# Optimization experiments

Measured on AMD Instinct MI355X. Metric: run time of the kernel, lower is better.

The kernel has to match this reference:

```python
import jax, jax.numpy as jnp
import numpy as np


def _pair_indices(num_emb):
    # pair (i, j), i != j; torch builds pair vector = concat(emb[j], emb[i])
    ii, jj = np.meshgrid(np.arange(num_emb), np.arange(num_emb), indexing='ij')
    mask = ii != jj
    return jnp.asarray(ii[mask]), jnp.asarray(jj[mask])


def setup_inputs() -> dict:
    key = jax.random.key(0)
    ks = jax.random.split(key, 8)
    B, n_way, n_shot, n_query, F = 64, 2, 6, 16, 512
    s = 0.02
    return {
        'x_shot_feat': jax.random.normal(ks[0], (B * n_way * n_shot, F), jnp.float32),
        'x_query_feat': jax.random.normal(ks[1], (B * n_query, F), jnp.float32),
        'Wg1': jax.random.normal(ks[2], (2 * F, F), jnp.float32) * s,
        'bg1': jnp.zeros((F,), jnp.float32),
        'Wg2': jax.random.normal(ks[3], (F, F), jnp.float32) * s,
        'bg2': jnp.zeros((F,), jnp.float32),
        'Wf1': jax.random.normal(ks[4], (F, F), jnp.float32) * s,
        'bf1': jnp.zeros((F,), jnp.float32),
        'Wf2': jax.random.normal(ks[5], (F, 1), jnp.float32) * s,
        'bf2': jnp.zeros((1,), jnp.float32),
        'batch_size': B, 'n_way': n_way, 'n_shot': n_shot, 'n_query': n_query,
    }


def reference(x_shot_feat, x_query_feat, Wg1, bg1, Wg2, bg2, Wf1, bf1, Wf2, bf2,
              batch_size, n_way, n_shot, n_query):
    F = x_shot_feat.shape[-1]
    num_emb = n_shot + 1
    x_shot = x_shot_feat.reshape(batch_size, n_way, n_shot, F)
    pos, neg = x_shot[:, 0], x_shot[:, 1]          # [B, n_shot, F]
    q = x_query_feat.reshape(batch_size, n_query, F)

    # emb: [B, Q, way=2, num_emb, F]  (support set + the single query appended)
    shot = jnp.stack([pos, neg], axis=1)           # [B, 2, n_shot, F]
    shot_b = jnp.broadcast_to(shot[:, None], (batch_size, n_query, 2, n_shot, F))
    q_b = jnp.broadcast_to(q[:, :, None, None, :], (batch_size, n_query, 2, 1, F))
    emb = jnp.concatenate([shot_b, q_b], axis=3)   # [B, Q, 2, num_emb, F]

    idx_i, idx_j = _pair_indices(num_emb)          # P = num_emb^2 - num_emb
    # pair(i,j) = concat(emb[j], emb[i])  (matches torch expand order)
    pairs = jnp.concatenate([emb[..., idx_j, :], emb[..., idx_i, :]], axis=-1)  # [B,Q,2,P,2F]

    g = jax.nn.relu(pairs @ Wg1 + bg1)
    g = jax.nn.relu(g @ Wg2 + bg2)                 # [B, Q, 2, P, F]
    s = jnp.sum(g, axis=3)                         # [B, Q, 2, F]
    logit = jax.nn.relu(s @ Wf1 + bf1) @ Wf2 + bf2 # [B, Q, 2, 1]
    return logit[..., 0]                           # [B, Q, n_way]
```

## Files before the change

kernel.cpp:

```cpp
#include <hip/hip_runtime.h>
#include <stdint.h>

typedef _Float16 f16x8 __attribute__((ext_vector_type(8)));
typedef float f32x4 __attribute__((ext_vector_type(4)));

__device__ __forceinline__ void gload16(const void* g, void* l) {
  __builtin_amdgcn_global_load_lds((const __attribute__((address_space(1))) void*)g,
                                   (__attribute__((address_space(3))) void*)l,
                                   16, 0, 0);
}

__device__ __forceinline__ void maprow_ss(int gr, int& rowU, int& rowV, bool& ok) {
  int g = gr >> 5, p = gr & 31;
  ok = (p < 30);
  int i = p / 5, jj = p % 5;
  int j = jj + (jj >= i);
  rowU = g * 6 + j;
  rowV = g * 6 + i;
  if (!ok) { rowU = 0; rowV = 0; }
}

__device__ __forceinline__ void maprow_sq(int gr, int& rowU, int& rowV) {
  int h = gr / 12, p = gr % 12;
  int b = h >> 5, q = (h >> 1) & 15, wv = h & 1;
  int sbase = (b * 2 + wv) * 6;
  int qrow = 768 + b * 16 + q;
  if (p < 6) { rowU = qrow; rowV = sbase + p; }
  else       { rowU = sbase + (p - 6); rowV = qrow; }
}

__device__ __forceinline__ f16x8 cvt8h(float4 a, float4 b) {
  f16x8 o;
  o[0] = (_Float16)a.x; o[1] = (_Float16)a.y; o[2] = (_Float16)a.z; o[3] = (_Float16)a.w;
  o[4] = (_Float16)b.x; o[5] = (_Float16)b.y; o[6] = (_Float16)b.z; o[7] = (_Float16)b.w;
  return o;
}

__global__ void convert_t(const float* __restrict__ Wg1, const float* __restrict__ Wg2,
                          const float* __restrict__ Wf1, const float* __restrict__ bf2,
                          _Float16* __restrict__ Wg1T, _Float16* __restrict__ Wg2T,
                          _Float16* __restrict__ Wf1T, float* __restrict__ out) {
  int tt = blockIdx.x * 256 + threadIdx.x;
  if (tt < 2048) out[tt] = bf2[0];
  const float* src;
  _Float16* dst;
  int c, k0, scol, srow0;
  if (tt < 65536) {
    c = tt & 1023; k0 = (tt >> 10) << 3;
    dst = Wg1T + (size_t)c * 512 + k0;
    if (c < 512) { src = Wg1; scol = c; srow0 = k0; }
    else         { src = Wg1; scol = c - 512; srow0 = 512 + k0; }
  } else if (tt < 98304) {
    int t2 = tt - 65536;
    c = t2 & 511; k0 = (t2 >> 9) << 3;
    dst = Wg2T + (size_t)c * 512 + k0;
    src = Wg2; scol = c; srow0 = k0;
  } else {
    int t3 = tt - 98304;
    c = t3 & 511; k0 = (t3 >> 9) << 3;
    dst = Wf1T + (size_t)c * 512 + k0;
    src = Wf1; scol = c; srow0 = k0;
  }
  f16x8 o;
#pragma unroll
  for (int i = 0; i < 8; i++)
    o[i] = (_Float16)src[(size_t)(srow0 + i) * 512 + scol];
  *(f16x8*)dst = o;
}

__global__ __launch_bounds__(256, 2) void gemm1_fused(
    const float* __restrict__ xs, const float* __restrict__ xq,
    const _Float16* __restrict__ BT, const float* __restrict__ bg1,
    _Float16* __restrict__ UVh) {
  __shared__ __align__(16) char smem[24576];

  int bid = blockIdx.x;
  { int q = gridDim.x >> 3; bid = (bid & 7) * q + (bid >> 3); }
  const int tm = bid >> 4;
  const int tn = bid & 15;
  const int t = threadIdx.x, w = t >> 6, l = t & 63;
  const int wm = (w >> 1) << 6, wn = (w & 1) << 5;
  const int lr = l & 15, lg = l >> 4;

  const int rl0 = t >> 2, c = t & 3;
  const int wchunk = c ^ ((rl0 >> 2) & 3);
  const int gr0 = tm * 128 + rl0, gr1 = gr0 + 64;
  const float* x0 = ((gr0 < 768) ? xs + (size_t)gr0 * 512 : xq + (size_t)(gr0 - 768) * 512) + c * 8;
  const float* x1 = ((gr1 < 768) ? xs + (size_t)gr1 * 512 : xq + (size_t)(gr1 - 768) * 512) + c * 8;

  const int kch = ((t & 3) ^ ((t >> 4) & 3)) * 8;
  const _Float16* Bg = BT + (size_t)(tn * 64 + rl0) * 512 + kch;

  _Float16* As_base = (_Float16*)smem;
  char*     Bs_base = smem + 16384;

  f32x4 acc[4][2];
#pragma unroll
  for (int m = 0; m < 4; m++)
#pragma unroll
    for (int n = 0; n < 2; n++) acc[m][n] = (f32x4){0.f, 0.f, 0.f, 0.f};
  const int rchunk = (lg ^ (lr >> 2)) * 8;

  gload16(Bg, Bs_base + t * 16);
  {
    float4 a0 = *(const float4*)(x0), a1 = *(const float4*)(x0 + 4);
    float4 b0 = *(const float4*)(x1), b1 = *(const float4*)(x1 + 4);
    *(f16x8*)(As_base + rl0 * 32 + wchunk * 8) = cvt8h(a0, a1);
    *(f16x8*)(As_base + (rl0 + 64) * 32 + wchunk * 8) = cvt8h(b0, b1);
  }
  __syncthreads();

  int cur = 0;
  for (int it = 0; it < 15; ++it) {
    const int nxt = cur ^ 1;
    const int kn = (it + 1) * 32;
    gload16(Bg + kn, Bs_base + nxt * 4096 + t * 16);
    float4 a0 = *(const float4*)(x0 + kn), a1 = *(const float4*)(x0 + kn + 4);
    float4 b0 = *(const float4*)(x1 + kn), b1 = *(const float4*)(x1 + kn + 4);
    {
      _Float16* As = As_base + cur * 4096;
      _Float16* Bs = (_Float16*)(Bs_base + cur * 4096);
      f16x8 fa[4], fb[2];
#pragma unroll
      for (int m = 0; m < 4; m++)
        fa[m] = *(const f16x8*)(As + (wm + m * 16 + lr) * 32 + rchunk);
#pragma unroll
      for (int n = 0; n < 2; n++)
        fb[n] = *(const f16x8*)(Bs + (wn + n * 16 + lr) * 32 + rchunk);
#pragma unroll
      for (int m = 0; m < 4; m++)
#pragma unroll
        for (int n = 0; n < 2; n++)
          acc[m][n] = __builtin_amdgcn_mfma_f32_16x16x32_f16(fa[m], fb[n], acc[m][n], 0, 0, 0);
    }
    *(f16x8*)(As_base + nxt * 4096 + rl0 * 32 + wchunk * 8) = cvt8h(a0, a1);
    *(f16x8*)(As_base + nxt * 4096 + (rl0 + 64) * 32 + wchunk * 8) = cvt8h(b0, b1);
    __syncthreads();
    cur = nxt;
  }
  {
    _Float16* As = As_base + cur * 4096;
    _Float16* Bs = (_Float16*)(Bs_base + cur * 4096);
    f16x8 fa[4], fb[2];
#pragma unroll
    for (int m = 0; m < 4; m++)
      fa[m] = *(const f16x8*)(As + (wm + m * 16 + lr) * 32 + rchunk);
#pragma unroll
    for (int n = 0; n < 2; n++)
      fb[n] = *(const f16x8*)(Bs + (wn + n * 16 + lr) * 32 + rchunk);
#pragma unroll
    for (int m = 0; m < 4; m++)
#pragma unroll
      for (int n = 0; n < 2; n++)
        acc[m][n] = __builtin_amdgcn_mfma_f32_16x16x32_f16(fa[m], fb[n], acc[m][n], 0, 0, 0);
  }

#pragma unroll
  for (int m = 0; m < 4; m++)
#pragma unroll
    for (int n = 0; n < 2; n++) {
      int col = tn * 64 + wn + n * 16 + lr;
      float bv = (col >= 512) ? bg1[col - 512] : 0.0f;
#pragma unroll
      for (int reg = 0; reg < 4; reg++) {
        int row = tm * 128 + wm + m * 16 + lg * 4 + reg;
        UVh[(size_t)row * 1024 + col] = (_Float16)(acc[m][n][reg] + bv);
      }
    }
}

__global__ __launch_bounds__(256, 2) void gemm2_fused(
    const _Float16* __restrict__ UVh,
    const _Float16* __restrict__ BT, const float* __restrict__ bg2,
    float* __restrict__ outSS, float* __restrict__ outSQ) {
  __shared__ __align__(16) char smem[32768];

  int bid = blockIdx.x;
  { int q = gridDim.x >> 3; bid = (bid & 7) * q + (bid >> 3); }
  const int t = threadIdx.x, w = t >> 6, l = t & 63;
  const int lr = l & 15, lg = l >> 4;
  const int rl = t >> 2, c = t & 3;
  const int wchunk = c ^ ((t >> 4) & 3);
  const int kch = ((t & 3) ^ ((t >> 4) & 3)) * 8;
  const int rchunk = (lg ^ (lr >> 2)) * 8;
  const f16x8 zz = {};
  char* Bsb = smem + 16384;

  if (bid < 1024) {
    const int tile = bid >> 2, tn = bid & 3;
    const int wm = (w >> 1) * 48, wn = (w & 1) << 6;

    int rU0, rV0, rU1 = 0, rV1 = 0;
    maprow_sq(tile * 96 + rl, rU0, rV0);
    if (t < 128) maprow_sq(tile * 96 + 64 + rl, rU1, rV1);
    const _Float16* u0p = UVh + (size_t)rU0 * 1024 + c * 8;
    const _Float16* v0p = UVh + (size_t)rV0 * 1024 + 512 + c * 8;
    const _Float16* u1p = UVh + (size_t)rU1 * 1024 + c * 8;
    const _Float16* v1p = UVh + (size_t)rV1 * 1024 + 512 + c * 8;
    const _Float16* Bg = BT + (size_t)(tn * 128 + rl) * 512 + kch;

    f32x4 acc[3][4];
#pragma unroll
    for (int m = 0; m < 3; m++)
#pragma unroll
      for (int n = 0; n < 4; n++) acc[m][n] = (f32x4){0.f, 0.f, 0.f, 0.f};

    {
      f16x8 u0 = *(const f16x8*)(u0p), v0 = *(const f16x8*)(v0p);
      *(f16x8*)((_Float16*)smem + rl * 32 + wchunk * 8) =
          __builtin_elementwise_max(u0 + v0, zz);
      if (t < 128) {
        f16x8 u1 = *(const f16x8*)(u1p), v1 = *(const f16x8*)(v1p);
        *(f16x8*)((_Float16*)smem + (64 + rl) * 32 + wchunk * 8) =
            __builtin_elementwise_max(u1 + v1, zz);
      }
    }
    gload16(Bg, Bsb + t * 16);
    gload16(Bg + (size_t)64 * 512, Bsb + 4096 + t * 16);
    __syncthreads();

    int cur = 0;
    for (int it = 0; it < 15; ++it) {
      const int nxt = cur ^ 1;
      const int kn = (it + 1) * 32;
      gload16(Bg + kn, Bsb + nxt * 8192 + t * 16);
      gload16(Bg + (size_t)64 * 512 + kn, Bsb + nxt * 8192 + 4096 + t * 16);
      f16x8 u0 = *(const f16x8*)(u0p + kn), v0 = *(const f16x8*)(v0p + kn);
      f16x8 u1, v1;
      if (t < 128) { u1 = *(const f16x8*)(u1p + kn); v1 = *(const f16x8*)(v1p + kn); }
      {
        _Float16* As = (_Float16*)(smem + cur * 6144);
        _Float16* Bs = (_Float16*)(Bsb + cur * 8192);
        f16x8 fa[3], fb[4];
#pragma unroll
        for (int m = 0; m < 3; m++)
          fa[m] = *(const f16x8*)(As + (wm + m * 16 + lr) * 32 + rchunk);
#pragma unroll
        for (int n = 0; n < 4; n++)
          fb[n] = *(const f16x8*)(Bs + (wn + n * 16 + lr) * 32 + rchunk);
#pragma unroll
        for (int m = 0; m < 3; m++)
#pragma unroll
          for (int n = 0; n < 4; n++)
            acc[m][n] = __builtin_amdgcn_mfma_f32_16x16x32_f16(fa[m], fb[n], acc[m][n], 0, 0, 0);
      }
      {
        _Float16* Aw = (_Float16*)(smem + nxt * 6144);
        *(f16x8*)(Aw + rl * 32 + wchunk * 8) = __builtin_elementwise_max(u0 + v0, zz);
        if (t < 128)
          *(f16x8*)(Aw + (64 + rl) * 32 + wchunk * 8) = __builtin_elementwise_max(u1 + v1, zz);
      }
      __syncthreads();
      cur = nxt;
    }
    {
      _Float16* As = (_Float16*)(smem + cur * 6144);
      _Float16* Bs = (_Float16*)(Bsb + cur * 8192);
      f16x8 fa[3], fb[4];
#pragma unroll
      for (int m = 0; m < 3; m++)
        fa[m] = *(const f16x8*)(As + (wm + m * 16 + lr) * 32 + rchunk);
#pragma unroll
      for (int n = 0; n < 4; n++)
        fb[n] = *(const f16x8*)(Bs + (wn + n * 16 + lr) * 32 + rchunk);
#pragma unroll
      for (int m = 0; m < 3; m++)
#pragma unroll
        for (int n = 0; n < 4; n++)
          acc[m][n] = __builtin_amdgcn_mfma_f32_16x16x32_f16(fa[m], fb[n], acc[m][n], 0, 0, 0);
    }
    __syncthreads();

    float* scr = (float*)smem + w * 192;
#pragma unroll
    for (int n = 0; n < 4; n++) {
      int col = tn * 128 + wn + n * 16 + lr;
      float bv = bg2[col];
#pragma unroll
      for (int m = 0; m < 3; m++) {
        float s = 0.0f;
#pragma unroll
        for (int reg = 0; reg < 4; reg++)
          s += fmaxf(acc[m][n][reg] + bv, 0.0f);
        scr[(4 * m + lg) * 16 + lr] = s;
      }
#pragma unroll
      for (int g = 0; g < 4; g++) {
        float vs = scr[(3 * g) * 16 + lr] + scr[(3 * g + 1) * 16 + lr] +
                   scr[(3 * g + 2) * 16 + lr];
        if (l < 16) {
          int hh = tile * 8 + ((wm == 48) ? 4 : 0) + g;
          outSQ[(size_t)hh * 512 + col] = vs;
        }
      }
    }
  } else {
    const int sbid = bid - 1024;
    const int tm = sbid >> 2, tn = sbid & 3;
    const int wm = (w >> 1) << 6, wn = (w & 1) << 6;

    int rU0, rV0, rU1, rV1; bool ok0, ok1;
    maprow_ss(tm * 128 + rl, rU0, rV0, ok0);
    maprow_ss(tm * 128 + rl + 64, rU1, rV1, ok1);
    const _Float16* u0p = UVh + (size_t)rU0 * 1024 + c * 8;
    const _Float16* v0p = UVh + (size_t)rV0 * 1024 + 512 + c * 8;
    const _Float16* u1p = UVh + (size_t)rU1 * 1024 + c * 8;
    const _Float16* v1p = UVh + (size_t)rV1 * 1024 + 512 + c * 8;
    const _Float16* Bg = BT + (size_t)(tn * 128 + rl) * 512 + kch;

    f32x4 acc[4][4];
#pragma unroll
    for (int m = 0; m < 4; m++)
#pragma unroll
      for (int n = 0; n < 4; n++) acc[m][n] = (f32x4){0.f, 0.f, 0.f, 0.f};

    {
      f16x8 u0 = *(const f16x8*)(u0p), v0 = *(const f16x8*)(v0p);
      f16x8 u1 = *(const f16x8*)(u1p), v1 = *(const f16x8*)(v1p);
      f16x8 o0 = ok0 ? __builtin_elementwise_max(u0 + v0, zz) : zz;
      f16x8 o1 = ok1 ? __builtin_elementwise_max(u1 + v1, zz) : zz;
      *(f16x8*)((_Float16*)smem + rl * 32 + wchunk * 8) = o0;
      *(f16x8*)((_Float16*)smem + (rl + 64) * 32 + wchunk * 8) = o1;
    }
    gload16(Bg, Bsb + t * 16);
    gload16(Bg + (size_t)64 * 512, Bsb + 4096 + t * 16);
    __syncthreads();

    int cur = 0;
    for (int it = 0; it < 15; ++it) {
      const int nxt = cur ^ 1;
      const int kn = (it + 1) * 32;
      gload16(Bg + kn, Bsb + nxt * 8192 + t * 16);
      gload16(Bg + (size_t)64 * 512 + kn, Bsb + nxt * 8192 + 4096 + t * 16);
      f16x8 u0 = *(const f16x8*)(u0p + kn), v0 = *(const f16x8*)(v0p + kn);
      f16x8 u1 = *(const f16x8*)(u1p + kn), v1 = *(const f16x8*)(v1p + kn);
      {
        _Float16* As = (_Float16*)(smem + cur * 8192);
        _Float16* Bs = (_Float16*)(Bsb + cur * 8192);
        f16x8 fa[4], fb[4];
#pragma unroll
        for (int m = 0; m < 4; m++)
          fa[m] = *(const f16x8*)(As + (wm + m * 16 + lr) * 32 + rchunk);
#pragma unroll
        for (int n = 0; n < 4; n++)
          fb[n] = *(const f16x8*)(Bs + (wn + n * 16 + lr) * 32 + rchunk);
#pragma unroll
        for (int m = 0; m < 4; m++)
#pragma unroll
          for (int n = 0; n < 4; n++)
            acc[m][n] = __builtin_amdgcn_mfma_f32_16x16x32_f16(fa[m], fb[n], acc[m][n], 0, 0, 0);
      }
      {
        f16x8 o0 = ok0 ? __builtin_elementwise_max(u0 + v0, zz) : zz;
        f16x8 o1 = ok1 ? __builtin_elementwise_max(u1 + v1, zz) : zz;
        _Float16* Aw = (_Float16*)(smem + nxt * 8192);
        *(f16x8*)(Aw + rl * 32 + wchunk * 8) = o0;
        *(f16x8*)(Aw + (rl + 64) * 32 + wchunk * 8) = o1;
      }
      __syncthreads();
      cur = nxt;
    }
    {
      _Float16* As = (_Float16*)(smem + cur * 8192);
      _Float16* Bs = (_Float16*)(Bsb + cur * 8192);
      f16x8 fa[4], fb[4];
#pragma unroll
      for (int m = 0; m < 4; m++)
        fa[m] = *(const f16x8*)(As + (wm + m * 16 + lr) * 32 + rchunk);
#pragma unroll
      for (int n = 0; n < 4; n++)
        fb[n] = *(const f16x8*)(Bs + (wn + n * 16 + lr) * 32 + rchunk);
#pragma unroll
      for (int m = 0; m < 4; m++)
#pragma unroll
        for (int n = 0; n < 4; n++)
          acc[m][n] = __builtin_amdgcn_mfma_f32_16x16x32_f16(fa[m], fb[n], acc[m][n], 0, 0, 0);
    }

#pragma unroll
    for (int pair = 0; pair < 2; pair++) {
#pragma unroll
      for (int n = 0; n < 4; n++) {
        int col = tn * 128 + wn + n * 16 + lr;
        float bv = bg2[col];
        float s = 0.0f;
#pragma unroll
        for (int mh = 0; mh < 2; mh++) {
          int m = pair * 2 + mh;
#pragma unroll
          for (int reg = 0; reg < 4; reg++) {
            bool ok = (mh == 0) || (lg * 4 + reg < 14);
            float v = fmaxf(acc[m][n][reg] + bv, 0.0f);
            s += ok ? v : 0.0f;
          }
        }
        s += __shfl_xor(s, 16);
        s += __shfl_xor(s, 32);
        if (l < 16) {
          int g = (wm >> 5) + pair;
          outSS[(size_t)(tm * 4 + g) * 512 + col] = s;
        }
      }
    }
  }
}

__global__ __launch_bounds__(256, 2) void gemm3_fused(
    const float* __restrict__ SS, const float* __restrict__ SQ,
    const _Float16* __restrict__ BT, const float* __restrict__ bf1,
    const float* __restrict__ Wf2, float* __restrict__ out) {
  __shared__ __align__(16) char smem[24576];

  int bid = blockIdx.x;
  { int q = gridDim.x >> 3; bid = (bid & 7) * q + (bid >> 3); }
  const int tm = bid >> 3;
  const int tn = bid & 7;
  const int t = threadIdx.x, w = t >> 6, l = t & 63;
  const int wm = (w >> 1) << 6, wn = (w & 1) << 5;
  const int lr = l & 15, lg = l >> 4;

  const int rl0 = t >> 2, c = t & 3;
  const int wchunk = c ^ ((rl0 >> 2) & 3);
  const int gr0 = tm * 128 + rl0, gr1 = gr0 + 64;
  const int ss0 = (gr0 >> 5) * 2 + (gr0 & 1);
  const int ss1 = (gr1 >> 5) * 2 + (gr1 & 1);
  const float* s0p = SS + (size_t)ss0 * 512 + c * 8;
  const float* q0p = SQ + (size_t)gr0 * 512 + c * 8;
  const float* s1p = SS + (size_t)ss1 * 512 + c * 8;
  const float* q1p = SQ + (size_t)gr1 * 512 + c * 8;

  const int kch = ((t & 3) ^ ((t >> 4) & 3)) * 8;
  const _Float16* Bg = BT + (size_t)(tn * 64 + rl0) * 512 + kch;

  _Float16* As_base = (_Float16*)smem;
  char*     Bs_base = smem + 16384;

  f32x4 acc[4][2];
#pragma unroll
  for (int m = 0; m < 4; m++)
#pragma unroll
    for (int n = 0; n < 2; n++) acc[m][n] = (f32x4){0.f, 0.f, 0.f, 0.f};
  const int rchunk = (lg ^ (lr >> 2)) * 8;

#define BUILD_S(o, a0, a1, b0, b1)                                           \
  {                                                                          \
    o[0] = (_Float16)(a0.x + b0.x); o[1] = (_Float16)(a0.y + b0.y);          \
    o[2] = (_Float16)(a0.z + b0.z); o[3] = (_Float16)(a0.w + b0.w);          \
    o[4] = (_Float16)(a1.x + b1.x); o[5] = (_Float16)(a1.y + b1.y);          \
    o[6] = (_Float16)(a1.z + b1.z); o[7] = (_Float16)(a1.w + b1.w);          \
  }

  gload16(Bg, Bs_base + t * 16);
  {
    float4 a0 = *(const float4*)(s0p), a1 = *(const float4*)(s0p + 4);
    float4 b0 = *(const float4*)(q0p), b1 = *(const float4*)(q0p + 4);
    float4 c0 = *(const float4*)(s1p), c1 = *(const float4*)(s1p + 4);
    float4 d0 = *(const float4*)(q1p), d1 = *(const float4*)(q1p + 4);
    f16x8 o0, o1;
    BUILD_S(o0, a0, a1, b0, b1);
    BUILD_S(o1, c0, c1, d0, d1);
    *(f16x8*)(As_base + rl0 * 32 + wchunk * 8) = o0;
    *(f16x8*)(As_base + (rl0 + 64) * 32 + wchunk * 8) = o1;
  }
  __syncthreads();

  int cur = 0;
  for (int it = 0; it < 15; ++it) {
    const int nxt = cur ^ 1;
    const int kn = (it + 1) * 32;
    gload16(Bg + kn, Bs_base + nxt * 4096 + t * 16);
    float4 a0 = *(const float4*)(s0p + kn), a1 = *(const float4*)(s0p + kn + 4);
    float4 b0 = *(const float4*)(q0p + kn), b1 = *(const float4*)(q0p + kn + 4);
    float4 c0 = *(const float4*)(s1p + kn), c1 = *(const float4*)(s1p + kn + 4);
    float4 d0 = *(const float4*)(q1p + kn), d1 = *(const float4*)(q1p + kn + 4);
    {
      _Float16* As = As_base + cur * 4096;
      _Float16* Bs = (_Float16*)(Bs_base + cur * 4096);
      f16x8 fa[4], fb[2];
#pragma unroll
      for (int m = 0; m < 4; m++)
        fa[m] = *(const f16x8*)(As + (wm + m * 16 + lr) * 32 + rchunk);
#pragma unroll
      for (int n = 0; n < 2; n++)
        fb[n] = *(const f16x8*)(Bs + (wn + n * 16 + lr) * 32 + rchunk);
#pragma unroll
      for (int m = 0; m < 4; m++)
#pragma unroll
        for (int n = 0; n < 2; n++)
          acc[m][n] = __builtin_amdgcn_mfma_f32_16x16x32_f16(fa[m], fb[n], acc[m][n], 0, 0, 0);
    }
    {
      f16x8 o0, o1;
      BUILD_S(o0, a0, a1, b0, b1);
      BUILD_S(o1, c0, c1, d0, d1);
      *(f16x8*)(As_base + nxt * 4096 + rl0 * 32 + wchunk * 8) = o0;
      *(f16x8*)(As_base + nxt * 4096 + (rl0 + 64) * 32 + wchunk * 8) = o1;
    }
    __syncthreads();
    cur = nxt;
  }
  {
    _Float16* As = As_base + cur * 4096;
    _Float16* Bs = (_Float16*)(Bs_base + cur * 4096);
    f16x8 fa[4], fb[2];
#pragma unroll
    for (int m = 0; m < 4; m++)
      fa[m] = *(const f16x8*)(As + (wm + m * 16 + lr) * 32 + rchunk);
#pragma unroll
    for (int n = 0; n < 2; n++)
      fb[n] = *(const f16x8*)(Bs + (wn + n * 16 + lr) * 32 + rchunk);
#pragma unroll
    for (int m = 0; m < 4; m++)
#pragma unroll
      for (int n = 0; n < 2; n++)
        acc[m][n] = __builtin_amdgcn_mfma_f32_16x16x32_f16(fa[m], fb[n], acc[m][n], 0, 0, 0);
  }

  float bf1v[2], wf2v[2];
#pragma unroll
  for (int n = 0; n < 2; n++) {
    int col = tn * 64 + wn + n * 16 + lr;
    bf1v[n] = bf1[col];
    wf2v[n] = Wf2[col];
  }
#pragma unroll
  for (int m = 0; m < 4; m++) {
#pragma unroll
    for (int reg = 0; reg < 4; reg++) {
      float p = 0.0f;
#pragma unroll
      for (int n = 0; n < 2; n++)
        p += fmaxf(acc[m][n][reg] + bf1v[n], 0.0f) * wf2v[n];
      p += __shfl_xor(p, 1);
      p += __shfl_xor(p, 2);
      p += __shfl_xor(p, 4);
      p += __shfl_xor(p, 8);
      if (lr == 0) {
        int row = tm * 128 + wm + m * 16 + lg * 4 + reg;
        atomicAdd(&out[row], p);
      }
    }
  }
#undef BUILD_S
}

extern "C" void kernel_launch(void* const* d_in, const int* in_sizes, int n_in,
                              void* d_out, int out_size, void* d_ws, size_t ws_size,
                              hipStream_t stream) {
  const float* xs  = (const float*)d_in[0];
  const float* xq  = (const float*)d_in[1];
  const float* Wg1 = (const float*)d_in[2];
  const float* bg1 = (const float*)d_in[3];
  const float* Wg2 = (const float*)d_in[4];
  const float* bg2 = (const float*)d_in[5];
  const float* Wf1 = (const float*)d_in[6];
  const float* bf1 = (const float*)d_in[7];
  const float* Wf2 = (const float*)d_in[8];
  const float* bf2 = (const float*)d_in[9];
  float* out = (float*)d_out;

  char* ws = (char*)d_ws;
  _Float16* Wg1T = (_Float16*)(ws);
  _Float16* Wg2T = (_Float16*)(ws + 1048576);
  _Float16* Wf1T = (_Float16*)(ws + 1572864);
  _Float16* UVh  = (_Float16*)(ws + 2097152);
  float*    SSs  = (float*)(ws + 5767168);
  float*    SQs  = (float*)(ws + 6029312);

  convert_t<<<512, 256, 0, stream>>>(Wg1, Wg2, Wf1, bf2, Wg1T, Wg2T, Wf1T, out);
  gemm1_fused<<<224, 256, 0, stream>>>(xs, xq, Wg1T, bg1, UVh);
  gemm2_fused<<<1152, 256, 0, stream>>>(UVh, Wg2T, bg2, SSs, SQs);
  gemm3_fused<<<128, 256, 0, stream>>>(SSs, SQs, Wf1T, bf1, Wf2, out);
}
```

Baseline: 71.93 us.

## Split gemm2 into separate SQ and SS kernels; build SQ A-fragments in registers

Splits the fused gemm2 kernel into two launches, one for support-query pairs and one for support-support pairs. In the SQ kernel each lane now loads its U and V rows straight into MFMA A-fragment registers and applies add+ReLU there, so the A tile no longer goes through LDS. The loads are prefetched one K-step ahead and a manual vmcnt/barrier sequence replaces __syncthreads. This cuts LDS traffic and halves the LDS footprint of the SQ path, which may improve occupancy. In exchange the two kernels now run back to back instead of sharing one grid, which adds a launch and a tail, and the hand-written waitcnt counts have to match the number of outstanding loads exactly.

```diff
diff --git a/kernel.cpp b/kernel.cpp
--- a/kernel.cpp
+++ b/kernel.cpp
@@ -169,16 +169,131 @@
     }
 }
 
-__global__ __launch_bounds__(256, 2) void gemm2_fused(
+__global__ __launch_bounds__(256, 2) void gemm2_sq(
     const _Float16* __restrict__ UVh,
     const _Float16* __restrict__ BT, const float* __restrict__ bg2,
-    float* __restrict__ outSS, float* __restrict__ outSQ) {
-  __shared__ __align__(16) char smem[32768];
+    float* __restrict__ outSQ) {
+  __shared__ __align__(16) char smem[16384];
 
   int bid = blockIdx.x;
   { int q = gridDim.x >> 3; bid = (bid & 7) * q + (bid >> 3); }
+  const int tile = bid >> 2, tn = bid & 3;
   const int t = threadIdx.x, w = t >> 6, l = t & 63;
   const int lr = l & 15, lg = l >> 4;
+  const int wm = (w >> 1) * 48, wn = (w & 1) << 6;
+  const int rl = t >> 2;
+  const int kch = ((t & 3) ^ ((t >> 4) & 3)) * 8;
+  const int rchunk = (lg ^ (lr >> 2)) * 8;
+  const f16x8 zz = {};
+
+  const _Float16 *uf[3], *vf[3];
+#pragma unroll
+  for (int m = 0; m < 3; m++) {
+    int rU, rV;
+    maprow_sq(tile * 96 + wm + m * 16 + lr, rU, rV);
+    uf[m] = UVh + (size_t)rU * 1024 + lg * 8;
+    vf[m] = UVh + (size_t)rV * 1024 + 512 + lg * 8;
+  }
+  const _Float16* Bg = BT + (size_t)(tn * 128 + rl) * 512 + kch;
+
+  f32x4 acc[3][4];
+#pragma unroll
+  for (int m = 0; m < 3; m++)
+#pragma unroll
+    for (int n = 0; n < 4; n++) acc[m][n] = (f32x4){0.f, 0.f, 0.f, 0.f};
+
+  gload16(Bg, smem + t * 16);
+  gload16(Bg + (size_t)64 * 512, smem + 4096 + t * 16);
+  f16x8 uc[3], vc[3];
+#pragma unroll
+  for (int m = 0; m < 3; m++) { uc[m] = *(const f16x8*)(uf[m]); vc[m] = *(const f16x8*)(vf[m]); }
+  asm volatile("s_waitcnt vmcnt(6) lgkmcnt(0)" ::: "memory");
+  __builtin_amdgcn_s_barrier();
+  asm volatile("" ::: "memory");
+
+  for (int it = 0; it < 15; ++it) {
+    const int kn = (it + 1) * 32;
+    const int nxt = (it + 1) & 1;
+    gload16(Bg + kn, smem + nxt * 8192 + t * 16);
+    gload16(Bg + (size_t)64 * 512 + kn, smem + nxt * 8192 + 4096 + t * 16);
+    f16x8 un[3], vn[3];
+#pragma unroll
+    for (int m = 0; m < 3; m++) { un[m] = *(const f16x8*)(uf[m] + kn); vn[m] = *(const f16x8*)(vf[m] + kn); }
+    {
+      _Float16* Bs = (_Float16*)(smem + (it & 1) * 8192);
+      f16x8 fb[4];
+#pragma unroll
+      for (int n = 0; n < 4; n++)
+        fb[n] = *(const f16x8*)(Bs + (wn + n * 16 + lr) * 32 + rchunk);
+      f16x8 fa[3];
+#pragma unroll
+      for (int m = 0; m < 3; m++) fa[m] = __builtin_elementwise_max(uc[m] + vc[m], zz);
+#pragma unroll
+      for (int m = 0; m < 3; m++)
+#pragma unroll
+        for (int n = 0; n < 4; n++)
+          acc[m][n] = __builtin_amdgcn_mfma_f32_16x16x32_f16(fa[m], fb[n], acc[m][n], 0, 0, 0);
+    }
+    asm volatile("s_waitcnt vmcnt(6) lgkmcnt(0)" ::: "memory");
+    __builtin_amdgcn_s_barrier();
+    asm volatile("" ::: "memory");
+#pragma unroll
+    for (int m = 0; m < 3; m++) { uc[m] = un[m]; vc[m] = vn[m]; }
+  }
+  {
+    _Float16* Bs = (_Float16*)(smem + 8192);
+    f16x8 fb[4];
+#pragma unroll
+    for (int n = 0; n < 4; n++)
+      fb[n] = *(const f16x8*)(Bs + (wn + n * 16 + lr) * 32 + rchunk);
+    f16x8 fa[3];
+#pragma unroll
+    for (int m = 0; m < 3; m++) fa[m] = __builtin_elementwise_max(uc[m] + vc[m], zz);
+#pragma unroll
+    for (int m = 0; m < 3; m++)
+#pragma unroll
+      for (int n = 0; n < 4; n++)
+        acc[m][n] = __builtin_amdgcn_mfma_f32_16x16x32_f16(fa[m], fb[n], acc[m][n], 0, 0, 0);
+  }
+  __syncthreads();
+
+  float* scr = (float*)smem + w * 192;
+#pragma unroll
+  for (int n = 0; n < 4; n++) {
+    int col = tn * 128 + wn + n * 16 + lr;
+    float bv = bg2[col];
+#pragma unroll
+    for (int m = 0; m < 3; m++) {
+      float s = 0.0f;
+#pragma unroll
+      for (int reg = 0; reg < 4; reg++)
+        s += fmaxf(acc[m][n][reg] + bv, 0.0f);
+      scr[(4 * m + lg) * 16 + lr] = s;
+    }
+#pragma unroll
+    for (int g = 0; g < 4; g++) {
+      float vs = scr[(3 * g) * 16 + lr] + scr[(3 * g + 1) * 16 + lr] +
+                 scr[(3 * g + 2) * 16 + lr];
+      if (l < 16) {
+        int hh = tile * 8 + ((wm == 48) ? 4 : 0) + g;
+        outSQ[(size_t)hh * 512 + col] = vs;
+      }
+    }
+  }
+}
+
+__global__ __launch_bounds__(256, 2) void gemm2_ss(
+    const _Float16* __restrict__ UVh,
+    const _Float16* __restrict__ BT, const float* __restrict__ bg2,
+    float* __restrict__ outSS) {
+  __shared__ __align__(16) char smem[32768];
+
+  int bid = blockIdx.x;
+  { int q = gridDim.x >> 3; bid = (bid & 7) * q + (bid >> 3); }
+  const int tm = bid >> 2, tn = bid & 3;
+  const int t = threadIdx.x, w = t >> 6, l = t & 63;
+  const int lr = l & 15, lg = l >> 4;
+  const int wm = (w >> 1) << 6, wn = (w & 1) << 6;
   const int rl = t >> 2, c = t & 3;
   const int wchunk = c ^ ((t >> 4) & 3);
   const int kch = ((t & 3) ^ ((t >> 4) & 3)) * 8;
@@ -186,180 +301,41 @@
   const f16x8 zz = {};
   char* Bsb = smem + 16384;
 
-  if (bid < 1024) {
-    const int tile = bid >> 2, tn = bid & 3;
-    const int wm = (w >> 1) * 48, wn = (w & 1) << 6;
-
-    int rU0, rV0, rU1 = 0, rV1 = 0;
-    maprow_sq(tile * 96 + rl, rU0, rV0);
-    if (t < 128) maprow_sq(tile * 96 + 64 + rl, rU1, rV1);
-    const _Float16* u0p = UVh + (size_t)rU0 * 1024 + c * 8;
-    const _Float16* v0p = UVh + (size_t)rV0 * 1024 + 512 + c * 8;
-    const _Float16* u1p = UVh + (size_t)rU1 * 1024 + c * 8;
-    const _Float16* v1p = UVh + (size_t)rV1 * 1024 + 512 + c * 8;
-    const _Float16* Bg = BT + (size_t)(tn * 128 + rl) * 512 + kch;
-
-    f32x4 acc[3][4];
-#pragma unroll
-    for (int m = 0; m < 3; m++)
-#pragma unroll
-      for (int n = 0; n < 4; n++) acc[m][n] = (f32x4){0.f, 0.f, 0.f, 0.f};
-
-    {
-      f16x8 u0 = *(const f16x8*)(u0p), v0 = *(const f16x8*)(v0p);
-      *(f16x8*)((_Float16*)smem + rl * 32 + wchunk * 8) =
-          __builtin_elementwise_max(u0 + v0, zz);
-      if (t < 128) {
-        f16x8 u1 = *(const f16x8*)(u1p), v1 = *(const f16x8*)(v1p);
-        *(f16x8*)((_Float16*)smem + (64 + rl) * 32 + wchunk * 8) =
-            __builtin_elementwise_max(u1 + v1, zz);
-      }
-    }
-    gload16(Bg, Bsb + t * 16);
-    gload16(Bg + (size_t)64 * 512, Bsb + 4096 + t * 16);
-    __syncthreads();
-
-    int cur = 0;
-    for (int it = 0; it < 15; ++it) {
-      const int nxt = cur ^ 1;
-      const int kn = (it + 1) * 32;
-      gload16(Bg + kn, Bsb + nxt * 8192 + t * 16);
-      gload16(Bg + (size_t)64 * 512 + kn, Bsb + nxt * 8192 + 4096 + t * 16);
-      f16x8 u0 = *(const f16x8*)(u0p + kn), v0 = *(const f16x8*)(v0p + kn);
-      f16x8 u1, v1;
-      if (t < 128) { u1 = *(const f16x8*)(u1p + kn); v1 = *(const f16x8*)(v1p + kn); }
-      {
-        _Float16* As = (_Float16*)(smem + cur * 6144);
-        _Float16* Bs = (_Float16*)(Bsb + cur * 8192);
-        f16x8 fa[3], fb[4];
-#pragma unroll
-        for (int m = 0; m < 3; m++)
-          fa[m] = *(const f16x8*)(As + (wm + m * 16 + lr) * 32 + rchunk);
-#pragma unroll
-        for (int n = 0; n < 4; n++)
-          fb[n] = *(const f16x8*)(Bs + (wn + n * 16 + lr) * 32 + rchunk);
-#pragma unroll
-        for (int m = 0; m < 3; m++)
-#pragma unroll
-          for (int n = 0; n < 4; n++)
-            acc[m][n] = __builtin_amdgcn_mfma_f32_16x16x32_f16(fa[m], fb[n], acc[m][n], 0, 0, 0);
-      }
-      {
-        _Float16* Aw = (_Float16*)(smem + nxt * 6144);
-        *(f16x8*)(Aw + rl * 32 + wchunk * 8) = __builtin_elementwise_max(u0 + v0, zz);
-        if (t < 128)
-          *(f16x8*)(Aw + (64 + rl) * 32 + wchunk * 8) = __builtin_elementwise_max(u1 + v1, zz);
-      }
-      __syncthreads();
-      cur = nxt;
-    }
-    {
-      _Float16* As = (_Float16*)(smem + cur * 6144);
-      _Float16* Bs = (_Float16*)(Bsb + cur * 8192);
-      f16x8 fa[3], fb[4];
-#pragma unroll
-      for (int m = 0; m < 3; m++)
-        fa[m] = *(const f16x8*)(As + (wm + m * 16 + lr) * 32 + rchunk);
-#pragma unroll
-      for (int n = 0; n < 4; n++)
-        fb[n] = *(const f16x8*)(Bs + (wn + n * 16 + lr) * 32 + rchunk);
-#pragma unroll
-      for (int m = 0; m < 3; m++)
-#pragma unroll
-        for (int n = 0; n < 4; n++)
-          acc[m][n] = __builtin_amdgcn_mfma_f32_16x16x32_f16(fa[m], fb[n], acc[m][n], 0, 0, 0);
-    }
-    __syncthreads();
-
-    float* scr = (float*)smem + w * 192;
-#pragma unroll
-    for (int n = 0; n < 4; n++) {
-      int col = tn * 128 + wn + n * 16 + lr;
-      float bv = bg2[col];
-#pragma unroll
-      for (int m = 0; m < 3; m++) {
-        float s = 0.0f;
-#pragma unroll
-        for (int reg = 0; reg < 4; reg++)
-          s += fmaxf(acc[m][n][reg] + bv, 0.0f);
-        scr[(4 * m + lg) * 16 + lr] = s;
-      }
-#pragma unroll
-      for (int g = 0; g < 4; g++) {
-        float vs = scr[(3 * g) * 16 + lr] + scr[(3 * g + 1) * 16 + lr] +
-                   scr[(3 * g + 2) * 16 + lr];
-        if (l < 16) {
-          int hh = tile * 8 + ((wm == 48) ? 4 : 0) + g;
-          outSQ[(size_t)hh * 512 + col] = vs;
-        }
-      }
-    }
-  } else {
-    const int sbid = bid - 1024;
-    const int tm = sbid >> 2, tn = sbid & 3;
-    const int wm = (w >> 1) << 6, wn = (w & 1) << 6;
-
-    int rU0, rV0, rU1, rV1; bool ok0, ok1;
-    maprow_ss(tm * 128 + rl, rU0, rV0, ok0);
-    maprow_ss(tm * 128 + rl + 64, rU1, rV1, ok1);
-    const _Float16* u0p = UVh + (size_t)rU0 * 1024 + c * 8;
-    const _Float16* v0p = UVh + (size_t)rV0 * 1024 + 512 + c * 8;
-    const _Float16* u1p = UVh + (size_t)rU1 * 1024 + c * 8;
-    const _Float16* v1p = UVh + (size_t)rV1 * 1024 + 512 + c * 8;
-    const _Float16* Bg = BT + (size_t)(tn * 128 + rl) * 512 + kch;
-
-    f32x4 acc[4][4];
-#pragma unroll
-    for (int m = 0; m < 4; m++)
-#pragma unroll
-      for (int n = 0; n < 4; n++) acc[m][n] = (f32x4){0.f, 0.f, 0.f, 0.f};
-
-    {
-      f16x8 u0 = *(const f16x8*)(u0p), v0 = *(const f16x8*)(v0p);
-      f16x8 u1 = *(const f16x8*)(u1p), v1 = *(const f16x8*)(v1p);
-      f16x8 o0 = ok0 ? __builtin_elementwise_max(u0 + v0, zz) : zz;
-      f16x8 o1 = ok1 ? __builtin_elementwise_max(u1 + v1, zz) : zz;
-      *(f16x8*)((_Float16*)smem + rl * 32 + wchunk * 8) = o0;
-      *(f16x8*)((_Float16*)smem + (rl + 64) * 32 + wchunk * 8) = o1;
-    }
-    gload16(Bg, Bsb + t * 16);
-    gload16(Bg + (size_t)64 * 512, Bsb + 4096 + t * 16);
-    __syncthreads();
-
-    int cur = 0;
-    for (int it = 0; it < 15; ++it) {
-      const int nxt = cur ^ 1;
-      const int kn = (it + 1) * 32;
-      gload16(Bg + kn, Bsb + nxt * 8192 + t * 16);
-      gload16(Bg + (size_t)64 * 512 + kn, Bsb + nxt * 8192 + 4096 + t * 16);
-      f16x8 u0 = *(const f16x8*)(u0p + kn), v0 = *(const f16x8*)(v0p + kn);
-      f16x8 u1 = *(const f16x8*)(u1p + kn), v1 = *(const f16x8*)(v1p + kn);
-      {
-        _Float16* As = (_Float16*)(smem + cur * 8192);
-        _Float16* Bs = (_Float16*)(Bsb + cur * 8192);
-        f16x8 fa[4], fb[4];
-#pragma unroll
-        for (int m = 0; m < 4; m++)
-          fa[m] = *(const f16x8*)(As + (wm + m * 16 + lr) * 32 + rchunk);
-#pragma unroll
-        for (int n = 0; n < 4; n++)
-          fb[n] = *(const f16x8*)(Bs + (wn + n * 16 + lr) * 32 + rchunk);
-#pragma unroll
-        for (int m = 0; m < 4; m++)
-#pragma unroll
-          for (int n = 0; n < 4; n++)
-            acc[m][n] = __builtin_amdgcn_mfma_f32_16x16x32_f16(fa[m], fb[n], acc[m][n], 0, 0, 0);
-      }
-      {
-        f16x8 o0 = ok0 ? __builtin_elementwise_max(u0 + v0, zz) : zz;
-        f16x8 o1 = ok1 ? __builtin_elementwise_max(u1 + v1, zz) : zz;
-        _Float16* Aw = (_Float16*)(smem + nxt * 8192);
-        *(f16x8*)(Aw + rl * 32 + wchunk * 8) = o0;
-        *(f16x8*)(Aw + (rl + 64) * 32 + wchunk * 8) = o1;
-      }
-      __syncthreads();
-      cur = nxt;
-    }
+  int rU0, rV0, rU1, rV1; bool ok0, ok1;
+  maprow_ss(tm * 128 + rl, rU0, rV0, ok0);
+  maprow_ss(tm * 128 + rl + 64, rU1, rV1, ok1);
+  const _Float16* u0p = UVh + (size_t)rU0 * 1024 + c * 8;
+  const _Float16* v0p = UVh + (size_t)rV0 * 1024 + 512 + c * 8;
+  const _Float16* u1p = UVh + (size_t)rU1 * 1024 + c * 8;
+  const _Float16* v1p = UVh + (size_t)rV1 * 1024 + 512 + c * 8;
+  const _Float16* Bg = BT + (size_t)(tn * 128 + rl) * 512 + kch;
+
+  f32x4 acc[4][4];
+#pragma unroll
+  for (int m = 0; m < 4; m++)
+#pragma unroll
+    for (int n = 0; n < 4; n++) acc[m][n] = (f32x4){0.f, 0.f, 0.f, 0.f};
+
+  {
+    f16x8 u0 = *(const f16x8*)(u0p), v0 = *(const f16x8*)(v0p);
+    f16x8 u1 = *(const f16x8*)(u1p), v1 = *(const f16x8*)(v1p);
+    f16x8 o0 = ok0 ? __builtin_elementwise_max(u0 + v0, zz) : zz;
+    f16x8 o1 = ok1 ? __builtin_elementwise_max(u1 + v1, zz) : zz;
+    *(f16x8*)((_Float16*)smem + rl * 32 + wchunk * 8) = o0;
+    *(f16x8*)((_Float16*)smem + (rl + 64) * 32 + wchunk * 8) = o1;
+  }
+  gload16(Bg, Bsb + t * 16);
+  gload16(Bg + (size_t)64 * 512, Bsb + 4096 + t * 16);
+  __syncthreads();
+
+  int cur = 0;
+  for (int it = 0; it < 15; ++it) {
+    const int nxt = cur ^ 1;
+    const int kn = (it + 1) * 32;
+    gload16(Bg + kn, Bsb + nxt * 8192 + t * 16);
+    gload16(Bg + (size_t)64 * 512 + kn, Bsb + nxt * 8192 + 4096 + t * 16);
+    f16x8 u0 = *(const f16x8*)(u0p + kn), v0 = *(const f16x8*)(v0p + kn);
+    f16x8 u1 = *(const f16x8*)(u1p + kn), v1 = *(const f16x8*)(v1p + kn);
     {
       _Float16* As = (_Float16*)(smem + cur * 8192);
       _Float16* Bs = (_Float16*)(Bsb + cur * 8192);
@@ -376,30 +352,55 @@
         for (int n = 0; n < 4; n++)
           acc[m][n] = __builtin_amdgcn_mfma_f32_16x16x32_f16(fa[m], fb[n], acc[m][n], 0, 0, 0);
     }
-
-#pragma unroll
-    for (int pair = 0; pair < 2; pair++) {
-#pragma unroll
-      for (int n = 0; n < 4; n++) {
-        int col = tn * 128 + wn + n * 16 + lr;
-        float bv = bg2[col];
-        float s = 0.0f;
-#pragma unroll
-        for (int mh = 0; mh < 2; mh++) {
-          int m = pair * 2 + mh;
-#pragma unroll
-          for (int reg = 0; reg < 4; reg++) {
-            bool ok = (mh == 0) || (lg * 4 + reg < 14);
-            float v = fmaxf(acc[m][n][reg] + bv, 0.0f);
-            s += ok ? v : 0.0f;
-          }
+    {
+      f16x8 o0 = ok0 ? __builtin_elementwise_max(u0 + v0, zz) : zz;
+      f16x8 o1 = ok1 ? __builtin_elementwise_max(u1 + v1, zz) : zz;
+      _Float16* Aw = (_Float16*)(smem + nxt * 8192);
+      *(f16x8*)(Aw + rl * 32 + wchunk * 8) = o0;
+      *(f16x8*)(Aw + (rl + 64) * 32 + wchunk * 8) = o1;
+    }
+    __syncthreads();
+    cur = nxt;
+  }
+  {
+    _Float16* As = (_Float16*)(smem + cur * 8192);
+    _Float16* Bs = (_Float16*)(Bsb + cur * 8192);
+    f16x8 fa[4], fb[4];
+#pragma unroll
+    for (int m = 0; m < 4; m++)
+      fa[m] = *(const f16x8*)(As + (wm + m * 16 + lr) * 32 + rchunk);
+#pragma unroll
+    for (int n = 0; n < 4; n++)
+      fb[n] = *(const f16x8*)(Bs + (wn + n * 16 + lr) * 32 + rchunk);
+#pragma unroll
+    for (int m = 0; m < 4; m++)
+#pragma unroll
+      for (int n = 0; n < 4; n++)
+        acc[m][n] = __builtin_amdgcn_mfma_f32_16x16x32_f16(fa[m], fb[n], acc[m][n], 0, 0, 0);
+  }
+
+#pragma unroll
+  for (int pair = 0; pair < 2; pair++) {
+#pragma unroll
+    for (int n = 0; n < 4; n++) {
+      int col = tn * 128 + wn + n * 16 + lr;
+      float bv = bg2[col];
+      float s = 0.0f;
+#pragma unroll
+      for (int mh = 0; mh < 2; mh++) {
+        int m = pair * 2 + mh;
+#pragma unroll
+        for (int reg = 0; reg < 4; reg++) {
+          bool ok = (mh == 0) || (lg * 4 + reg < 14);
+          float v = fmaxf(acc[m][n][reg] + bv, 0.0f);
+          s += ok ? v : 0.0f;
         }
-        s += __shfl_xor(s, 16);
-        s += __shfl_xor(s, 32);
-        if (l < 16) {
-          int g = (wm >> 5) + pair;
-          outSS[(size_t)(tm * 4 + g) * 512 + col] = s;
-        }
+      }
+      s += __shfl_xor(s, 16);
+      s += __shfl_xor(s, 32);
+      if (l < 16) {
+        int g = (wm >> 5) + pair;
+        outSS[(size_t)(tm * 4 + g) * 512 + col] = s;
       }
     }
   }
@@ -569,6 +570,7 @@
 
   convert_t<<<512, 256, 0, stream>>>(Wg1, Wg2, Wf1, bf2, Wg1T, Wg2T, Wf1T, out);
   gemm1_fused<<<224, 256, 0, stream>>>(xs, xq, Wg1T, bg1, UVh);
-  gemm2_fused<<<1152, 256, 0, stream>>>(UVh, Wg2T, bg2, SSs, SQs);
+  gemm2_sq<<<1024, 256, 0, stream>>>(UVh, Wg2T, bg2, SQs);
+  gemm2_ss<<<128, 256, 0, stream>>>(UVh, Wg2T, bg2, SSs);
   gemm3_fused<<<128, 256, 0, stream>>>(SSs, SQs, Wf1T, bf1, Wf2, out);
 }
```

Result: slower. 90.70 us (+26.1%).
